# Optimization experiments

Hardware: AMD Instinct MI355X
Metric: run time of the kernel (lower is better)

## Reference

```python
import jax, jax.numpy as jnp
import numpy as np

N, C, A, H, O, T = 18, 4, 14, 20, 8, 5  # nodes, classes, alarms, hidden, out, time steps


def _lin(key, dout, din, std):
    W = std * jax.random.normal(key, (dout, din), jnp.float32)
    b = jnp.zeros((dout,), jnp.float32)
    return W, b


def setup_inputs():
    key = jax.random.key(0)
    ks = jax.random.split(key, 12)
    adj = (jax.random.uniform(ks[0], (N, N)) < 0.3).astype(jnp.float32)  # binary adjacency
    x = jax.random.normal(ks[1], (N, H), jnp.float32)
    Wz, bz = _lin(ks[2], H, 2 * H, 0.1)
    Uz, buz = _lin(ks[3], H, H, 0.1)
    Wr, br = _lin(ks[4], H, 2 * H, 0.1)
    Ur, bur = _lin(ks[5], H, H, 0.1)
    Ww, bw = _lin(ks[6], H, 2 * H, 0.1)
    Uw, bu = _lin(ks[7], H, H, 0.1)
    Wo, bo = _lin(ks[8], O, 2 * H, 0.1)
    Wx, bx = _lin(ks[9], O, H, 0.01)
    Wy, by = _lin(ks[10], O, H, 0.01)
    w2, b2 = _lin(ks[11], 1, O, 0.1)
    return {"x": x, "adj": adj, "Wz": Wz, "bz": bz, "Uz": Uz, "buz": buz,
            "Wr": Wr, "br": br, "Ur": Ur, "bur": bur, "Ww": Ww, "bw": bw,
            "Uw": Uw, "bu": bu, "Wo": Wo, "bo": bo, "Wx": Wx, "bx": bx,
            "Wy": Wy, "by": by, "w2": w2, "b2": b2}


def reference(x, adj, Wz, bz, Uz, buz, Wr, br, Ur, bur, Ww, bw, Uw, bu,
              Wo, bo, Wx, bx, Wy, by, w2, b2):
    in_mat, out_mat = adj, adj.T  # split_matrix: in=A, out=A^T

    def step(h, _):
        # message aggregation over in/out edges, then GRU gates (eqs 3-5)
        a = jnp.concatenate([in_mat @ h, out_mat @ h], axis=1)        # [N, 2H]
        z = jax.nn.sigmoid(a @ Wz.T + bz + h @ Uz.T + buz)            # update gate
        r = jax.nn.sigmoid(a @ Wr.T + br + h @ Ur.T + bur)            # reset gate
        hg = jnp.tanh(a @ Ww.T + bw + (r * h) @ Uw.T + bu)            # candidate
        return (1.0 - z) * h + z * hg, None

    h, _ = jax.lax.scan(step, x, None, length=T)                       # [N, H]
    out = jnp.tanh(jnp.concatenate([h, x], axis=1) @ Wo.T + bo)        # [N, O]

    # attention-style reasoning between class nodes and alarm nodes
    cfcx = jnp.tanh(h[:C] @ Wx.T + bx)                                 # [C, O]
    afcy = jnp.tanh(h[C:] @ Wy.T + by)                                 # [A, O]
    cacat = cfcx[:, None, :] * afcy[None, :, :]                        # [C, A, O]
    rfc = jax.nn.sigmoid(jnp.einsum('cao,o->ca', cacat, w2[0]) + b2[0])[..., None]
    mask = in_mat[:C, C:][..., None]                                   # [C, A, 1]
    rfc = rfc * mask

    weighted = out[C:][None, :, :] * rfc                               # [C, A, O]
    final = jnp.concatenate([out[:C][:, None, :], weighted], axis=1)   # [C, 1+A, O]
    return final
```

## Files before the change

kernel.cpp:

```cpp
#include <hip/hip_runtime.h>


__device__ __forceinline__ float fsig(float x){ return 1.0f/(1.0f+__expf(-x)); }
__device__ __forceinline__ float ftnh(float x){ return 1.0f - 2.0f/(__expf(2.0f*x)+1.0f); }

__global__ __launch_bounds__(768, 1) void ggnn_fused(
    const float* __restrict__ x,  const float* __restrict__ adj,
    const float* __restrict__ Wz, const float* __restrict__ bz,
    const float* __restrict__ Uz, const float* __restrict__ buz,
    const float* __restrict__ Wr, const float* __restrict__ br,
    const float* __restrict__ Ur, const float* __restrict__ bur,
    const float* __restrict__ Ww, const float* __restrict__ bw,
    const float* __restrict__ Uw, const float* __restrict__ bu,
    const float* __restrict__ Wo, const float* __restrict__ bo,
    const float* __restrict__ Wx, const float* __restrict__ bx,
    const float* __restrict__ Wy, const float* __restrict__ by,
    const float* __restrict__ w2, const float* __restrict__ b2,
    float* __restrict__ outp)
{
  __shared__ float sAdj[324];
  __shared__ float hA[360], hB[360];
  __shared__ float aaT[720];
  __shared__ float rrT[360], ws1[360];
  __shared__ float sOut[144], sCf[32], sAf[112], sRfc[56];

  const int tid = threadIdx.x;

  const int g    = (tid >> 6) & 1;
  const int idx  = (tid >> 7) * 64 + (tid & 63);
  const bool act2 = (idx < 360);
  const int i2 = idx / 18, n2 = idx % 18;

  const bool act1 = (tid < 720);
  const int n1 = tid % 18;
  const int kk = tid / 18;
  const int k1 = kk % 20;
  const int abase = (kk < 20) ? (n1 * 18) : n1;
  const int astep = (kk < 20) ? 1 : 18;

  if (tid < 324) sAdj[tid] = adj[tid];
  if (tid < 360) { int j = tid/18, n = tid%18; hA[j*18+n] = x[n*20+j]; }

  float4 w4[10], u4[5], wh4[5], uw4[5];
  float bias1 = 0.f, bwi = 0.f, bui = 0.f;
  if (act2) {
    const float* Wg = g ? Wr : Wz;
    const float* Ug = g ? Ur : Uz;
    #pragma unroll
    for (int q=0;q<10;q++) w4[q] = *(const float4*)(Wg + i2*40 + 4*q);
    #pragma unroll
    for (int q=0;q<5;q++){
      u4[q]  = *(const float4*)(Ug + i2*20 + 4*q);
      wh4[q] = *(const float4*)(Ww + i2*40 + g*20 + 4*q);
    }
    if (g == 0){
      bias1 = bz[i2] + buz[i2];
      bwi   = bw[i2];
      bui   = bu[i2];
      #pragma unroll
      for (int q=0;q<5;q++) uw4[q] = *(const float4*)(Uw + i2*20 + 4*q);
    } else {
      bias1 = br[i2] + bur[i2];
    }
  }
  __syncthreads();

  float* hc = hA;
  float* hn = hB;
  float zreg = 0.f, sw0 = 0.f;

  for (int t=0;t<5;t++){
    if (act1){
      float s = 0.f;
      #pragma unroll
      for (int m=0;m<18;m++) s += sAdj[abase + m*astep] * hc[k1*18+m];
      aaT[kk*18 + n1] = s;
    }
    __syncthreads();

    if (act2){
      float sg = bias1, sw = bwi;
      #pragma unroll
      for (int q=0;q<10;q++){
        float a0 = aaT[(4*q+0)*18+n2];
        float a1 = aaT[(4*q+1)*18+n2];
        float a2 = aaT[(4*q+2)*18+n2];
        float a3 = aaT[(4*q+3)*18+n2];
        sg += w4[q].x*a0 + w4[q].y*a1 + w4[q].z*a2 + w4[q].w*a3;
        if (g==0 && q<5)  { sw += wh4[q].x*a0 + wh4[q].y*a1 + wh4[q].z*a2 + wh4[q].w*a3; }
        if (g==1 && q>=5) { const float4 W = wh4[q-5]; sw += W.x*a0 + W.y*a1 + W.z*a2 + W.w*a3; }
      }
      #pragma unroll
      for (int q=0;q<5;q++){
        float h0 = hc[(4*q+0)*18+n2];
        float h1 = hc[(4*q+1)*18+n2];
        float h2 = hc[(4*q+2)*18+n2];
        float h3 = hc[(4*q+3)*18+n2];
        sg += u4[q].x*h0 + u4[q].y*h1 + u4[q].z*h2 + u4[q].w*h3;
      }
      if (g == 0){
        zreg = fsig(sg);
        sw0  = sw;
      } else {
        rrT[i2*18+n2] = fsig(sg);
        ws1[i2*18+n2] = sw;
      }
    }
    __syncthreads();

    if (g == 0 && act2){
      float s = bui + sw0 + ws1[i2*18+n2];
      #pragma unroll
      for (int q=0;q<5;q++){
        float u0=u4[0].x;
        (void)u0;
        s += uw4[q].x * rrT[(4*q+0)*18+n2] * hc[(4*q+0)*18+n2];
        s += uw4[q].y * rrT[(4*q+1)*18+n2] * hc[(4*q+1)*18+n2];
        s += uw4[q].z * rrT[(4*q+2)*18+n2] * hc[(4*q+2)*18+n2];
        s += uw4[q].w * rrT[(4*q+3)*18+n2] * hc[(4*q+3)*18+n2];
      }
      float hg = ftnh(s);
      hn[i2*18+n2] = (1.f - zreg)*hc[i2*18+n2] + zreg*hg;
    }
    __syncthreads();
    float* tmp = hc; hc = hn; hn = tmp;
  }

  if (tid < 144){
    int n_ = tid/8, o = tid%8;
    float s = bo[o];
    #pragma unroll
    for (int q=0;q<5;q++){
      float4 w = *(const float4*)(Wo + o*40 + 4*q);
      s += w.x*hc[(4*q+0)*18+n_] + w.y*hc[(4*q+1)*18+n_]
         + w.z*hc[(4*q+2)*18+n_] + w.w*hc[(4*q+3)*18+n_];
    }
    #pragma unroll
    for (int q=0;q<5;q++){
      float4 w  = *(const float4*)(Wo + o*40 + 20 + 4*q);
      float4 xv = *(const float4*)(x + n_*20 + 4*q);
      s += w.x*xv.x + w.y*xv.y + w.z*xv.z + w.w*xv.w;
    }
    sOut[tid] = ftnh(s);
  } else if (tid >= 192 && tid < 224){
    int ii = tid-192; int c = ii/8, o = ii%8;
    float s = bx[o];
    #pragma unroll
    for (int q=0;q<5;q++){
      float4 w = *(const float4*)(Wx + o*20 + 4*q);
      s += w.x*hc[(4*q+0)*18+c] + w.y*hc[(4*q+1)*18+c]
         + w.z*hc[(4*q+2)*18+c] + w.w*hc[(4*q+3)*18+c];
    }
    sCf[ii] = ftnh(s);
  } else if (tid >= 256 && tid < 368){
    int ii = tid-256; int a = ii/8, o = ii%8;
    float s = by[o];
    #pragma unroll
    for (int q=0;q<5;q++){
      float4 w = *(const float4*)(Wy + o*20 + 4*q);
      s += w.x*hc[(4*q+0)*18+4+a] + w.y*hc[(4*q+1)*18+4+a]
         + w.z*hc[(4*q+2)*18+4+a] + w.w*hc[(4*q+3)*18+4+a];
    }
    sAf[ii] = ftnh(s);
  }
  __syncthreads();

  if (tid < 56){
    int c = tid/14, a = tid%14;
    float4 w20 = *(const float4*)(w2);
    float4 w21 = *(const float4*)(w2+4);
    const float* cf = &sCf[c*8];
    const float* af = &sAf[a*8];
    float s = b2[0];
    s += cf[0]*af[0]*w20.x + cf[1]*af[1]*w20.y + cf[2]*af[2]*w20.z + cf[3]*af[3]*w20.w;
    s += cf[4]*af[4]*w21.x + cf[5]*af[5]*w21.y + cf[6]*af[6]*w21.z + cf[7]*af[7]*w21.w;
    sRfc[tid] = fsig(s) * sAdj[c*18 + 4 + a];
  }
  __syncthreads();

  if (tid < 480){
    int c = tid/120, rem = tid%120, s_ = rem/8, o = rem%8;
    float v = (s_ == 0) ? sOut[c*8+o]
                        : sOut[(3+s_)*8+o] * sRfc[c*14 + (s_-1)];
    outp[tid] = v;
  }
}

extern "C" void kernel_launch(void* const* d_in, const int* in_sizes, int n_in,
                              void* d_out, int out_size, void* d_ws, size_t ws_size,
                              hipStream_t stream) {
  (void)in_sizes; (void)n_in; (void)d_ws; (void)ws_size; (void)out_size;
  const float* x   = (const float*)d_in[0];
  const float* adj = (const float*)d_in[1];
  const float* Wz  = (const float*)d_in[2];
  const float* bz  = (const float*)d_in[3];
  const float* Uz  = (const float*)d_in[4];
  const float* buz = (const float*)d_in[5];
  const float* Wr  = (const float*)d_in[6];
  const float* br  = (const float*)d_in[7];
  const float* Ur  = (const float*)d_in[8];
  const float* bur = (const float*)d_in[9];
  const float* Ww  = (const float*)d_in[10];
  const float* bw  = (const float*)d_in[11];
  const float* Uw  = (const float*)d_in[12];
  const float* bu  = (const float*)d_in[13];
  const float* Wo  = (const float*)d_in[14];
  const float* bo  = (const float*)d_in[15];
  const float* Wx  = (const float*)d_in[16];
  const float* bx  = (const float*)d_in[17];
  const float* Wy  = (const float*)d_in[18];
  const float* by  = (const float*)d_in[19];
  const float* w2  = (const float*)d_in[20];
  const float* b2  = (const float*)d_in[21];
  float* outp = (float*)d_out;

  ggnn_fused<<<1, 768, 0, stream>>>(x, adj, Wz, bz, Uz, buz, Wr, br, Ur, bur,
                                    Ww, bw, Uw, bu, Wo, bo, Wx, bx, Wy, by,
                                    w2, b2, outp);
}
```

Before: 20.22 us.

## Halve block size, compute all gates per thread with node-major float4 layout

Switches hidden state and aggregation buffers from feature-major to node-major layout so the GRU loops can use float4 shared-memory loads. Each of 360 threads now computes the z, r and candidate sums for one (feature, node) pair, removing the cross-group exchange buffer, and the block shrinks from 768 to 384 threads. Aggregation holds each thread's adjacency row or column in registers and produces four features at once. In exchange each thread carries far more weight registers, which may raise register pressure and lengthen per-thread serial work on the critical path.

```diff
diff --git a/kernel.cpp b/kernel.cpp
--- a/kernel.cpp
+++ b/kernel.cpp
@@ -1,10 +1,12 @@
 #include <hip/hip_runtime.h>
 
+
+#define AS 44
 
 __device__ __forceinline__ float fsig(float x){ return 1.0f/(1.0f+__expf(-x)); }
 __device__ __forceinline__ float ftnh(float x){ return 1.0f - 2.0f/(__expf(2.0f*x)+1.0f); }
 
-__global__ __launch_bounds__(768, 1) void ggnn_fused(
+__global__ __launch_bounds__(384, 1) void ggnn_fused(
     const float* __restrict__ x,  const float* __restrict__ adj,
     const float* __restrict__ Wz, const float* __restrict__ bz,
     const float* __restrict__ Uz, const float* __restrict__ buz,
@@ -18,157 +20,157 @@
     const float* __restrict__ w2, const float* __restrict__ b2,
     float* __restrict__ outp)
 {
+  __shared__ __align__(16) float hA[360], hB[360];
+  __shared__ __align__(16) float aaL[18*AS];
+  __shared__ __align__(16) float rrL[360];
   __shared__ float sAdj[324];
-  __shared__ float hA[360], hB[360];
-  __shared__ float aaT[720];
-  __shared__ float rrT[360], ws1[360];
-  __shared__ float sOut[144], sCf[32], sAf[112], sRfc[56];
+  __shared__ __align__(16) float sOut[144], sCf[32], sAf[112], sRfc[56];
 
   const int tid = threadIdx.x;
 
-  const int g    = (tid >> 6) & 1;
-  const int idx  = (tid >> 7) * 64 + (tid & 63);
-  const bool act2 = (idx < 360);
-  const int i2 = idx / 18, n2 = idx % 18;
-
-  const bool act1 = (tid < 720);
-  const int n1 = tid % 18;
-  const int kk = tid / 18;
-  const int k1 = kk % 20;
-  const int abase = (kk < 20) ? (n1 * 18) : n1;
-  const int astep = (kk < 20) ? 1 : 18;
-
+  const bool act2 = (tid < 360);
+  const int i2 = tid / 18;
+  const int n2 = tid % 18;
+
+  const bool act1 = (tid < 180);
+  const int n1 = tid / 10;
+  const int q1 = tid % 10;
+  const int hoff1 = 4 * (q1 % 5);
+
+  if (tid < 90) ((float4*)hA)[tid] = ((const float4*)x)[tid];
   if (tid < 324) sAdj[tid] = adj[tid];
-  if (tid < 360) { int j = tid/18, n = tid%18; hA[j*18+n] = x[n*20+j]; }
-
-  float4 w4[10], u4[5], wh4[5], uw4[5];
-  float bias1 = 0.f, bwi = 0.f, bui = 0.f;
+
+  float adjv[18];
+  if (act1) {
+    #pragma unroll
+    for (int m = 0; m < 18; ++m)
+      adjv[m] = (q1 < 5) ? adj[n1*18 + m] : adj[m*18 + n1];
+  }
+
+  float4 wz4[10], wr4[10], ww4[10], uz4[5], ur4[5], uw4[5];
+  float bzz=0.f, brr=0.f, bww=0.f, bui=0.f;
   if (act2) {
-    const float* Wg = g ? Wr : Wz;
-    const float* Ug = g ? Ur : Uz;
-    #pragma unroll
-    for (int q=0;q<10;q++) w4[q] = *(const float4*)(Wg + i2*40 + 4*q);
-    #pragma unroll
-    for (int q=0;q<5;q++){
-      u4[q]  = *(const float4*)(Ug + i2*20 + 4*q);
-      wh4[q] = *(const float4*)(Ww + i2*40 + g*20 + 4*q);
-    }
-    if (g == 0){
-      bias1 = bz[i2] + buz[i2];
-      bwi   = bw[i2];
-      bui   = bu[i2];
-      #pragma unroll
-      for (int q=0;q<5;q++) uw4[q] = *(const float4*)(Uw + i2*20 + 4*q);
-    } else {
-      bias1 = br[i2] + bur[i2];
-    }
+    #pragma unroll
+    for (int q=0;q<10;q++){
+      wz4[q] = ((const float4*)(Wz + i2*40))[q];
+      wr4[q] = ((const float4*)(Wr + i2*40))[q];
+      ww4[q] = ((const float4*)(Ww + i2*40))[q];
+    }
+    #pragma unroll
+    for (int q=0;q<5;q++){
+      uz4[q] = ((const float4*)(Uz + i2*20))[q];
+      ur4[q] = ((const float4*)(Ur + i2*20))[q];
+      uw4[q] = ((const float4*)(Uw + i2*20))[q];
+    }
+    bzz = bz[i2] + buz[i2];
+    brr = br[i2] + bur[i2];
+    bww = bw[i2];
+    bui = bu[i2];
   }
   __syncthreads();
 
   float* hc = hA;
   float* hn = hB;
-  float zreg = 0.f, sw0 = 0.f;
-
-  for (int t=0;t<5;t++){
-    if (act1){
-      float s = 0.f;
-      #pragma unroll
-      for (int m=0;m<18;m++) s += sAdj[abase + m*astep] * hc[k1*18+m];
-      aaT[kk*18 + n1] = s;
+  float zreg = 0.f, swreg = 0.f;
+
+  for (int t = 0; t < 5; ++t) {
+    if (act1) {
+      float4 acc = make_float4(0.f,0.f,0.f,0.f);
+      #pragma unroll
+      for (int m = 0; m < 18; ++m) {
+        float4 h4 = *(const float4*)&hc[m*20 + hoff1];
+        float av = adjv[m];
+        acc.x += av*h4.x; acc.y += av*h4.y; acc.z += av*h4.z; acc.w += av*h4.w;
+      }
+      *(float4*)&aaL[n1*AS + 4*q1] = acc;
     }
     __syncthreads();
 
-    if (act2){
-      float sg = bias1, sw = bwi;
+    if (act2) {
+      float sz = bzz, sr = brr, sw = bww;
+      const float4* ar = (const float4*)&aaL[n2*AS];
       #pragma unroll
       for (int q=0;q<10;q++){
-        float a0 = aaT[(4*q+0)*18+n2];
-        float a1 = aaT[(4*q+1)*18+n2];
-        float a2 = aaT[(4*q+2)*18+n2];
-        float a3 = aaT[(4*q+3)*18+n2];
-        sg += w4[q].x*a0 + w4[q].y*a1 + w4[q].z*a2 + w4[q].w*a3;
-        if (g==0 && q<5)  { sw += wh4[q].x*a0 + wh4[q].y*a1 + wh4[q].z*a2 + wh4[q].w*a3; }
-        if (g==1 && q>=5) { const float4 W = wh4[q-5]; sw += W.x*a0 + W.y*a1 + W.z*a2 + W.w*a3; }
-      }
+        float4 a4 = ar[q];
+        sz += wz4[q].x*a4.x + wz4[q].y*a4.y + wz4[q].z*a4.z + wz4[q].w*a4.w;
+        sr += wr4[q].x*a4.x + wr4[q].y*a4.y + wr4[q].z*a4.z + wr4[q].w*a4.w;
+        sw += ww4[q].x*a4.x + ww4[q].y*a4.y + ww4[q].z*a4.z + ww4[q].w*a4.w;
+      }
+      const float4* hr = (const float4*)&hc[n2*20];
       #pragma unroll
       for (int q=0;q<5;q++){
-        float h0 = hc[(4*q+0)*18+n2];
-        float h1 = hc[(4*q+1)*18+n2];
-        float h2 = hc[(4*q+2)*18+n2];
-        float h3 = hc[(4*q+3)*18+n2];
-        sg += u4[q].x*h0 + u4[q].y*h1 + u4[q].z*h2 + u4[q].w*h3;
-      }
-      if (g == 0){
-        zreg = fsig(sg);
-        sw0  = sw;
-      } else {
-        rrT[i2*18+n2] = fsig(sg);
-        ws1[i2*18+n2] = sw;
-      }
+        float4 h4 = hr[q];
+        sz += uz4[q].x*h4.x + uz4[q].y*h4.y + uz4[q].z*h4.z + uz4[q].w*h4.w;
+        sr += ur4[q].x*h4.x + ur4[q].y*h4.y + ur4[q].z*h4.z + ur4[q].w*h4.w;
+      }
+      zreg  = fsig(sz);
+      swreg = sw;
+      rrL[n2*20 + i2] = fsig(sr);
     }
     __syncthreads();
 
-    if (g == 0 && act2){
-      float s = bui + sw0 + ws1[i2*18+n2];
+    if (act2) {
+      float s = swreg + bui;
+      const float4* rr4 = (const float4*)&rrL[n2*20];
+      const float4* hr  = (const float4*)&hc[n2*20];
       #pragma unroll
       for (int q=0;q<5;q++){
-        float u0=u4[0].x;
-        (void)u0;
-        s += uw4[q].x * rrT[(4*q+0)*18+n2] * hc[(4*q+0)*18+n2];
-        s += uw4[q].y * rrT[(4*q+1)*18+n2] * hc[(4*q+1)*18+n2];
-        s += uw4[q].z * rrT[(4*q+2)*18+n2] * hc[(4*q+2)*18+n2];
-        s += uw4[q].w * rrT[(4*q+3)*18+n2] * hc[(4*q+3)*18+n2];
+        float4 r4 = rr4[q];
+        float4 h4 = hr[q];
+        s += uw4[q].x*r4.x*h4.x + uw4[q].y*r4.y*h4.y
+           + uw4[q].z*r4.z*h4.z + uw4[q].w*r4.w*h4.w;
       }
       float hg = ftnh(s);
-      hn[i2*18+n2] = (1.f - zreg)*hc[i2*18+n2] + zreg*hg;
+      float hv = hc[n2*20 + i2];
+      hn[n2*20 + i2] = (1.f - zreg)*hv + zreg*hg;
     }
     __syncthreads();
     float* tmp = hc; hc = hn; hn = tmp;
   }
 
-  if (tid < 144){
+  if (tid < 144) {
     int n_ = tid/8, o = tid%8;
+    const float4* hr = (const float4*)&hc[n_*20];
+    const float4* wo = (const float4*)(Wo + o*40);
+    const float4* xv = (const float4*)(x + n_*20);
     float s = bo[o];
     #pragma unroll
     for (int q=0;q<5;q++){
-      float4 w = *(const float4*)(Wo + o*40 + 4*q);
-      s += w.x*hc[(4*q+0)*18+n_] + w.y*hc[(4*q+1)*18+n_]
-         + w.z*hc[(4*q+2)*18+n_] + w.w*hc[(4*q+3)*18+n_];
-    }
-    #pragma unroll
-    for (int q=0;q<5;q++){
-      float4 w  = *(const float4*)(Wo + o*40 + 20 + 4*q);
-      float4 xv = *(const float4*)(x + n_*20 + 4*q);
-      s += w.x*xv.x + w.y*xv.y + w.z*xv.z + w.w*xv.w;
+      float4 w = wo[q],  h4 = hr[q];
+      s += w.x*h4.x + w.y*h4.y + w.z*h4.z + w.w*h4.w;
+      float4 w2_ = wo[5+q], x4 = xv[q];
+      s += w2_.x*x4.x + w2_.y*x4.y + w2_.z*x4.z + w2_.w*x4.w;
     }
     sOut[tid] = ftnh(s);
-  } else if (tid >= 192 && tid < 224){
-    int ii = tid-192; int c = ii/8, o = ii%8;
+  } else if (tid >= 144 && tid < 176) {
+    int ii = tid-144; int c = ii/8, o = ii%8;
+    const float4* hr = (const float4*)&hc[c*20];
+    const float4* wx = (const float4*)(Wx + o*20);
     float s = bx[o];
     #pragma unroll
     for (int q=0;q<5;q++){
-      float4 w = *(const float4*)(Wx + o*20 + 4*q);
-      s += w.x*hc[(4*q+0)*18+c] + w.y*hc[(4*q+1)*18+c]
-         + w.z*hc[(4*q+2)*18+c] + w.w*hc[(4*q+3)*18+c];
+      float4 w = wx[q], h4 = hr[q];
+      s += w.x*h4.x + w.y*h4.y + w.z*h4.z + w.w*h4.w;
     }
     sCf[ii] = ftnh(s);
-  } else if (tid >= 256 && tid < 368){
-    int ii = tid-256; int a = ii/8, o = ii%8;
+  } else if (tid >= 176 && tid < 288) {
+    int ii = tid-176; int a = ii/8, o = ii%8;
+    const float4* hr = (const float4*)&hc[(4+a)*20];
+    const float4* wy = (const float4*)(Wy + o*20);
     float s = by[o];
     #pragma unroll
     for (int q=0;q<5;q++){
-      float4 w = *(const float4*)(Wy + o*20 + 4*q);
-      s += w.x*hc[(4*q+0)*18+4+a] + w.y*hc[(4*q+1)*18+4+a]
-         + w.z*hc[(4*q+2)*18+4+a] + w.w*hc[(4*q+3)*18+4+a];
+      float4 w = wy[q], h4 = hr[q];
+      s += w.x*h4.x + w.y*h4.y + w.z*h4.z + w.w*h4.w;
     }
     sAf[ii] = ftnh(s);
   }
   __syncthreads();
 
-  if (tid < 56){
+  if (tid < 56) {
     int c = tid/14, a = tid%14;
-    float4 w20 = *(const float4*)(w2);
-    float4 w21 = *(const float4*)(w2+4);
+    float4 w20 = ((const float4*)w2)[0];
+    float4 w21 = ((const float4*)w2)[1];
     const float* cf = &sCf[c*8];
     const float* af = &sAf[a*8];
     float s = b2[0];
@@ -178,11 +180,11 @@
   }
   __syncthreads();
 
-  if (tid < 480){
-    int c = tid/120, rem = tid%120, s_ = rem/8, o = rem%8;
-    float v = (s_ == 0) ? sOut[c*8+o]
-                        : sOut[(3+s_)*8+o] * sRfc[c*14 + (s_-1)];
-    outp[tid] = v;
+  for (int o = tid; o < 480; o += 384) {
+    int c = o/120, rem = o%120, s_ = rem/8, oo = rem%8;
+    float v = (s_ == 0) ? sOut[c*8+oo]
+                        : sOut[(3+s_)*8+oo] * sRfc[c*14 + (s_-1)];
+    outp[o] = v;
   }
 }
 
@@ -214,7 +216,7 @@
   const float* b2  = (const float*)d_in[21];
   float* outp = (float*)d_out;
 
-  ggnn_fused<<<1, 768, 0, stream>>>(x, adj, Wz, bz, Uz, buz, Wr, br, Ur, bur,
+  ggnn_fused<<<1, 384, 0, stream>>>(x, adj, Wz, bz, Uz, buz, Wr, br, Ur, bur,
                                     Ww, bw, Uw, bu, Wo, bo, Wx, bx, Wy, by,
                                     w2, b2, outp);
 }
```

Result: slower. 23.80 us (+17.7%).
